# Kernel optimization log

Hardware: AMD Instinct MI355X
Metric: run time of the kernel (lower is better)

## Reference

```python
import jax, jax.numpy as jnp
import numpy as np

B, K, L, D = 16, 64, 128, 768  # batch, top_k, max_length, embedding_dim


def setup_inputs() -> dict:
    key = jax.random.key(0)
    context = jax.random.normal(key, (B, K, 2, L, D), dtype=jnp.float32)
    return {"context": context}


def reference(context):
    # context: [B, K, 2, L, D]; slot 0 = mention context tokens, slot 1 = entity tokens
    ctx = context[:, :, 0]  # [B, K, L, D]
    ent = context[:, :, 1]  # [B, K, L, D]
    # token-token similarity per (batch, candidate): [B, K, L, L]
    sim = jnp.einsum("bkld,bkmd->bklm", ctx, ent)
    # per-context-token best entity token (hard argmax, non-differentiable index)
    idx = jnp.argmax(sim, axis=-1)  # [B, K, L] int
    # gather matched entity vectors: [B, K, L, D]
    ent_matched = jnp.take_along_axis(ent, idx[..., None], axis=2)
    # dot product per token then sum over tokens -> sum-of-max score [B, K]
    out = jnp.sum(ctx * ent_matched, axis=(-2, -1))
    return out
```

## Files before the change

### kernel.cpp

```cpp
#include <hip/hip_runtime.h>


typedef __attribute__((ext_vector_type(8))) __bf16 bf16x8;
typedef __attribute__((ext_vector_type(4))) __bf16 bf16x4;
typedef __attribute__((ext_vector_type(4))) float f32x4;

#define L_DIM 128
#define D_DIM 768
#define DC    64
#define LDP   72

__global__ __launch_bounds__(256, 4)
void som_kernel(const float* __restrict__ context, float* __restrict__ out) {
    const int bk   = blockIdx.x;
    const int t    = threadIdx.x;
    const int lane = t & 63;
    const int wave = t >> 6;
    const int quad = (lane >> 4) & 3;
    const int l15  = lane & 15;

    const float* ctx_g = context + (size_t)bk * (2 * L_DIM * D_DIM);
    const float* ent_g = ctx_g + (size_t)(L_DIM * D_DIM);

    __shared__ __bf16 ctx_s[L_DIM * LDP];
    __shared__ __bf16 ent_s[L_DIM * LDP];
    __shared__ float wave_sum[4];

    f32x4 acc[2][8];
    const f32x4 zero = {0.f, 0.f, 0.f, 0.f};
#pragma unroll
    for (int rt = 0; rt < 2; ++rt)
#pragma unroll
        for (int ct = 0; ct < 8; ++ct)
            acc[rt][ct] = zero;

    for (int c = 0; c < D_DIM / DC; ++c) {
        __syncthreads();
#pragma unroll 2
        for (int i = 0; i < 8; ++i) {
            const int g   = t + i * 256;
            const int row = g >> 4;
            const int c4  = g & 15;
            const int goff = row * D_DIM + c * DC + c4 * 4;
            const float4 vc = *(const float4*)(ctx_g + goff);
            const float4 ve = *(const float4*)(ent_g + goff);
            bf16x4 pc = {(__bf16)vc.x, (__bf16)vc.y, (__bf16)vc.z, (__bf16)vc.w};
            bf16x4 pe = {(__bf16)ve.x, (__bf16)ve.y, (__bf16)ve.z, (__bf16)ve.w};
            *(bf16x4*)&ctx_s[row * LDP + c4 * 4] = pc;
            *(bf16x4*)&ent_s[row * LDP + c4 * 4] = pe;
        }
        __syncthreads();

#pragma unroll
        for (int ks = 0; ks < 2; ++ks) {
            const bf16x8 a0 = *(const bf16x8*)&ctx_s[(wave * 32 + l15) * LDP + ks * 32 + quad * 8];
            const bf16x8 a1 = *(const bf16x8*)&ctx_s[(wave * 32 + 16 + l15) * LDP + ks * 32 + quad * 8];
#pragma unroll
            for (int ct = 0; ct < 8; ++ct) {
                const bf16x8 b = *(const bf16x8*)&ent_s[(ct * 16 + l15) * LDP + ks * 32 + quad * 8];
                acc[0][ct] = __builtin_amdgcn_mfma_f32_16x16x32_bf16(a0, b, acc[0][ct], 0, 0, 0);
                acc[1][ct] = __builtin_amdgcn_mfma_f32_16x16x32_bf16(a1, b, acc[1][ct], 0, 0, 0);
            }
        }
    }

    float total = 0.f;
#pragma unroll
    for (int rt = 0; rt < 2; ++rt) {
#pragma unroll
        for (int reg = 0; reg < 4; ++reg) {
            float m = acc[rt][0][reg];
#pragma unroll
            for (int ct = 1; ct < 8; ++ct) m = fmaxf(m, acc[rt][ct][reg]);
            m = fmaxf(m, __shfl_xor(m, 1, 64));
            m = fmaxf(m, __shfl_xor(m, 2, 64));
            m = fmaxf(m, __shfl_xor(m, 4, 64));
            m = fmaxf(m, __shfl_xor(m, 8, 64));
            total += m;
        }
    }
    total += __shfl_xor(total, 16, 64);
    total += __shfl_xor(total, 32, 64);

    if (lane == 0) wave_sum[wave] = total;
    __syncthreads();
    if (t == 0)
        out[bk] = wave_sum[0] + wave_sum[1] + wave_sum[2] + wave_sum[3];
}

extern "C" void kernel_launch(void* const* d_in, const int* in_sizes, int n_in,
                              void* d_out, int out_size, void* d_ws, size_t ws_size,
                              hipStream_t stream) {
    const float* context = (const float*)d_in[0];
    float* out = (float*)d_out;
    som_kernel<<<dim3(1024), dim3(256), 0, stream>>>(context, out);
}
```

Baseline: 1.000 ms.

## Double-buffer LDS chunks with register prefetch and use 8 waves per block

Doubles the block to 512 threads so each of 8 waves computes 16 context rows instead of 32. Shared-memory tiles are double-buffered: the next D-chunk is loaded from global into registers while the current chunk's MFMAs run, then converted and stored into the other buffer, leaving one barrier per chunk instead of two. This is meant to hide global-load latency behind compute in a memory-bound kernel. The cost is twice the LDS per block (about 72KB), which lowers the number of resident blocks per CU, and each B-fragment read now feeds only one MFMA.

Result: no change. 992.3 us (-0.8%).

```diff
diff --git a/kernel.cpp b/kernel.cpp
--- a/kernel.cpp
+++ b/kernel.cpp
@@ -8,9 +8,10 @@
 #define L_DIM 128
 #define D_DIM 768
 #define DC    64
+#define NCHUNK (D_DIM / DC)
 #define LDP   72
 
-__global__ __launch_bounds__(256, 4)
+__global__ __launch_bounds__(512, 4)
 void som_kernel(const float* __restrict__ context, float* __restrict__ out) {
     const int bk   = blockIdx.x;
     const int t    = threadIdx.x;
@@ -22,70 +23,99 @@
     const float* ctx_g = context + (size_t)bk * (2 * L_DIM * D_DIM);
     const float* ent_g = ctx_g + (size_t)(L_DIM * D_DIM);
 
-    __shared__ __bf16 ctx_s[L_DIM * LDP];
-    __shared__ __bf16 ent_s[L_DIM * LDP];
-    __shared__ float wave_sum[4];
+    __shared__ __bf16 ctx_s[2][L_DIM * LDP];
+    __shared__ __bf16 ent_s[2][L_DIM * LDP];
+    __shared__ float wave_sum[8];
 
-    f32x4 acc[2][8];
+    const int row0 = t >> 4;
+    const int c4   = t & 15;
+    const float* gc = ctx_g + row0 * D_DIM + c4 * 4;
+    const float* ge = ent_g + row0 * D_DIM + c4 * 4;
+    const int lds0 = row0 * LDP + c4 * 4;
+
+    f32x4 acc[8];
     const f32x4 zero = {0.f, 0.f, 0.f, 0.f};
 #pragma unroll
-    for (int rt = 0; rt < 2; ++rt)
+    for (int ct = 0; ct < 8; ++ct) acc[ct] = zero;
+
+    float4 pc[4], pe[4];
+
 #pragma unroll
-        for (int ct = 0; ct < 8; ++ct)
-            acc[rt][ct] = zero;
+    for (int i = 0; i < 4; ++i) {
+        pc[i] = *(const float4*)(gc + i * 32 * D_DIM);
+        pe[i] = *(const float4*)(ge + i * 32 * D_DIM);
+    }
+#pragma unroll
+    for (int i = 0; i < 4; ++i) {
+        bf16x4 qc = {(__bf16)pc[i].x, (__bf16)pc[i].y, (__bf16)pc[i].z, (__bf16)pc[i].w};
+        bf16x4 qe = {(__bf16)pe[i].x, (__bf16)pe[i].y, (__bf16)pe[i].z, (__bf16)pe[i].w};
+        *(bf16x4*)&ctx_s[0][lds0 + i * 32 * LDP] = qc;
+        *(bf16x4*)&ent_s[0][lds0 + i * 32 * LDP] = qe;
+    }
+    __syncthreads();
 
-    for (int c = 0; c < D_DIM / DC; ++c) {
-        __syncthreads();
-#pragma unroll 2
-        for (int i = 0; i < 8; ++i) {
-            const int g   = t + i * 256;
-            const int row = g >> 4;
-            const int c4  = g & 15;
-            const int goff = row * D_DIM + c * DC + c4 * 4;
-            const float4 vc = *(const float4*)(ctx_g + goff);
-            const float4 ve = *(const float4*)(ent_g + goff);
-            bf16x4 pc = {(__bf16)vc.x, (__bf16)vc.y, (__bf16)vc.z, (__bf16)vc.w};
-            bf16x4 pe = {(__bf16)ve.x, (__bf16)ve.y, (__bf16)ve.z, (__bf16)ve.w};
-            *(bf16x4*)&ctx_s[row * LDP + c4 * 4] = pc;
-            *(bf16x4*)&ent_s[row * LDP + c4 * 4] = pe;
+    for (int c = 0; c < NCHUNK; ++c) {
+        const int cur = c & 1;
+
+        if (c < NCHUNK - 1) {
+            const int base = (c + 1) * DC;
+#pragma unroll
+            for (int i = 0; i < 4; ++i) {
+                pc[i] = *(const float4*)(gc + i * 32 * D_DIM + base);
+                pe[i] = *(const float4*)(ge + i * 32 * D_DIM + base);
+            }
+        }
+
+        {
+            const __bf16* cs = ctx_s[cur];
+            const __bf16* es = ent_s[cur];
+#pragma unroll
+            for (int ks = 0; ks < 2; ++ks) {
+                const bf16x8 a = *(const bf16x8*)&cs[(wave * 16 + l15) * LDP + ks * 32 + quad * 8];
+#pragma unroll
+                for (int ct = 0; ct < 8; ++ct) {
+                    const bf16x8 b = *(const bf16x8*)&es[(ct * 16 + l15) * LDP + ks * 32 + quad * 8];
+                    acc[ct] = __builtin_amdgcn_mfma_f32_16x16x32_bf16(a, b, acc[ct], 0, 0, 0);
+                }
+            }
+        }
+
+        if (c < NCHUNK - 1) {
+            const int nxt = cur ^ 1;
+#pragma unroll
+            for (int i = 0; i < 4; ++i) {
+                bf16x4 qc = {(__bf16)pc[i].x, (__bf16)pc[i].y, (__bf16)pc[i].z, (__bf16)pc[i].w};
+                bf16x4 qe = {(__bf16)pe[i].x, (__bf16)pe[i].y, (__bf16)pe[i].z, (__bf16)pe[i].w};
+                *(bf16x4*)&ctx_s[nxt][lds0 + i * 32 * LDP] = qc;
+                *(bf16x4*)&ent_s[nxt][lds0 + i * 32 * LDP] = qe;
+            }
         }
         __syncthreads();
-
-#pragma unroll
-        for (int ks = 0; ks < 2; ++ks) {
-            const bf16x8 a0 = *(const bf16x8*)&ctx_s[(wave * 32 + l15) * LDP + ks * 32 + quad * 8];
-            const bf16x8 a1 = *(const bf16x8*)&ctx_s[(wave * 32 + 16 + l15) * LDP + ks * 32 + quad * 8];
-#pragma unroll
-            for (int ct = 0; ct < 8; ++ct) {
-                const bf16x8 b = *(const bf16x8*)&ent_s[(ct * 16 + l15) * LDP + ks * 32 + quad * 8];
-                acc[0][ct] = __builtin_amdgcn_mfma_f32_16x16x32_bf16(a0, b, acc[0][ct], 0, 0, 0);
-                acc[1][ct] = __builtin_amdgcn_mfma_f32_16x16x32_bf16(a1, b, acc[1][ct], 0, 0, 0);
-            }
-        }
     }
 
     float total = 0.f;
 #pragma unroll
-    for (int rt = 0; rt < 2; ++rt) {
+    for (int reg = 0; reg < 4; ++reg) {
+        float m = acc[0][reg];
 #pragma unroll
-        for (int reg = 0; reg < 4; ++reg) {
-            float m = acc[rt][0][reg];
-#pragma unroll
-            for (int ct = 1; ct < 8; ++ct) m = fmaxf(m, acc[rt][ct][reg]);
-            m = fmaxf(m, __shfl_xor(m, 1, 64));
-            m = fmaxf(m, __shfl_xor(m, 2, 64));
-            m = fmaxf(m, __shfl_xor(m, 4, 64));
-            m = fmaxf(m, __shfl_xor(m, 8, 64));
-            total += m;
-        }
+        for (int ct = 1; ct < 8; ++ct) m = fmaxf(m, acc[ct][reg]);
+        m = fmaxf(m, __shfl_xor(m, 1, 64));
+        m = fmaxf(m, __shfl_xor(m, 2, 64));
+        m = fmaxf(m, __shfl_xor(m, 4, 64));
+        m = fmaxf(m, __shfl_xor(m, 8, 64));
+        total += m;
     }
     total += __shfl_xor(total, 16, 64);
     total += __shfl_xor(total, 32, 64);
 
     if (lane == 0) wave_sum[wave] = total;
     __syncthreads();
-    if (t == 0)
-        out[bk] = wave_sum[0] + wave_sum[1] + wave_sum[2] + wave_sum[3];
+    if (t == 0) {
+        float s = 0.f;
+#pragma unroll
+        for (int w = 0; w < 8; ++w) s += wave_sum[w];
+        out[bk] = s;
+    }
 }
 
 extern "C" void kernel_launch(void* const* d_in, const int* in_sizes, int n_in,
@@ -93,5 +123,5 @@
                               hipStream_t stream) {
     const float* context = (const float*)d_in[0];
     float* out = (float*)d_out;
-    som_kernel<<<dim3(1024), dim3(256), 0, stream>>>(context, out);
+    som_kernel<<<dim3(1024), dim3(512), 0, stream>>>(context, out);
 }
```
